# Optimization experiments

Hardware: AMD Instinct MI355X
Metric: run time of the kernel (lower is better)

Reference implementation:

```python
import jax, jax.numpy as jnp
import numpy as np

B, C, H, W = 4, 64, 128, 128
NP = 9        # num_param (N offset points per pixel)
OUTC = 128
STRIDE = 1
EPS = 1e-5    # BatchNorm eps


def _conv(x, w, b=None, stride=1):
    out = jax.lax.conv_general_dilated(
        x, w, (stride, stride), 'SAME',
        dimension_numbers=('NCHW', 'OIHW', 'NCHW'))
    if b is not None:
        out = out + b[None, :, None, None]
    return out


def setup_inputs() -> dict:
    key = jax.random.key(0)
    ks = jax.random.split(key, 6)
    s = lambda k, sh, sc: jax.random.normal(k, sh, jnp.float32) * sc
    return dict(
        x=s(ks[0], (B, C, H, W), 1.0),
        p_w=s(ks[1], (2 * NP, C, 3, 3), 0.02),   # offset conv (3x3, pad 1)
        p_b=s(ks[2], (2 * NP,), 0.02),
        conv_w=s(ks[3], (OUTC, C, 1, 1), 0.05),  # final 1x1 conv, no bias
        bn_gamma=jnp.ones((OUTC,), jnp.float32),
        bn_beta=jnp.zeros((OUTC,), jnp.float32),
        attn_w=s(ks[4], (1, C, 1, 1), 0.05),
        attn_b=s(ks[5], (1,), 0.05),
    )


def _forward(x, p_w, p_b, conv_w, bn_gamma, bn_beta, attn_w, attn_b):
    N = NP
    # density attention (computed as in source; adaptive re-parameterization skipped)
    density = jax.nn.sigmoid(_conv(x, attn_w, attn_b))  # noqa: F841

    # learned offsets: [B, 2N, H, W] (first N channels = row/x, last N = col/y)
    offset = _conv(x, p_w, p_b, stride=STRIDE)

    # p_n: base kernel grid offsets (row-major 3x3 -> values 0..2)
    base_int = int(round(np.sqrt(NP)))
    row_number = NP // base_int
    ii, jj = np.meshgrid(np.arange(row_number), np.arange(base_int), indexing='ij')
    p_n = jnp.asarray(np.concatenate([ii.ravel(), jj.ravel()]).astype(np.float32))  # [2N]

    # p_0: per-pixel base coordinates
    p0x = jnp.broadcast_to(jnp.arange(H, dtype=jnp.float32)[:, None] * STRIDE, (H, W))
    p0y = jnp.broadcast_to(jnp.arange(W, dtype=jnp.float32)[None, :] * STRIDE, (H, W))
    p_0 = jnp.concatenate([jnp.broadcast_to(p0x, (N, H, W)),
                           jnp.broadcast_to(p0y, (N, H, W))], axis=0)  # [2N,H,W]

    # sampling locations p: [B, H, W, 2N]
    p = (offset + p_n[None, :, None, None] + p_0[None]).transpose(0, 2, 3, 1)

    q_lt = jax.lax.stop_gradient(jnp.floor(p))   # detached, as in source
    q_rb = q_lt + 1.0
    px, py = p[..., :N], p[..., N:]
    ltx, lty = q_lt[..., :N], q_lt[..., N:]
    rbx, rby = q_rb[..., :N], q_rb[..., N:]

    # bilinear weights
    g_lt = (1 + (ltx - px)) * (1 + (lty - py))
    g_rb = (1 - (rbx - px)) * (1 - (rby - py))
    g_lb = (1 + (ltx - px)) * (1 - (rby - py))
    g_rt = (1 - (rbx - px)) * (1 + (lty - py))

    HW = H * W
    x_flat = x.reshape(B, C, HW)

    def gather(qx, qy):
        idx = jnp.clip((qx * W + qy).astype(jnp.int32), 0, HW - 1)  # [B,H,W,N]
        idx = idx.reshape(B, -1)
        out = jax.vmap(lambda xf, ix: xf[:, ix])(x_flat, idx)       # [B,C,H*W*N]
        return out.reshape(B, C, H, W, N)

    x_off = (g_lt[:, None] * gather(ltx, lty)
             + g_rb[:, None] * gather(rbx, rby)
             + g_lb[:, None] * gather(ltx, rby)
             + g_rt[:, None] * gather(rbx, lty))    # [B,C,H,W,N]

    # rearrange 'b c h w n -> b c (h n) w'
    x_off = x_off.transpose(0, 1, 2, 4, 3).reshape(B, C, H * N, W)

    # 1x1 conv (no bias) + BatchNorm2d (training-mode batch stats) + SiLU
    y = _conv(x_off, conv_w)
    mean = y.mean(axis=(0, 2, 3))
    var = y.var(axis=(0, 2, 3))  # biased, as torch BN uses for normalization
    y = (y - mean[None, :, None, None]) * jax.lax.rsqrt(var[None, :, None, None] + EPS)
    y = y * bn_gamma[None, :, None, None] + bn_beta[None, :, None, None]
    return jax.nn.silu(y)


def reference(x, p_w, p_b, conv_w, bn_gamma, bn_beta, attn_w, attn_b):
    return _forward(x, p_w, p_b, conv_w, bn_gamma, bn_beta, attn_w, attn_b)
```

## Files before the change

kernel.cpp:

```cpp
#include <hip/hip_runtime.h>

#define CIN   64
#define NOUT  128
#define IMH   128
#define IMW   128
#define NPTS  9
#define NB    4
#define HW    (IMH*IMW)
#define ROWS  (IMH*NPTS)
#define CHS   (ROWS*IMW)
#define TOTAL ((size_t)NB*NOUT*CHS)

typedef float f32x4 __attribute__((ext_vector_type(4)));

__global__ __launch_bounds__(256) void k_offset(const float* __restrict__ x,
                                                const float* __restrict__ pw,
                                                const float* __restrict__ pb,
                                                float* __restrict__ off,
                                                float* __restrict__ stats0) {
    __shared__ float wl[576 * 20];
    __shared__ float red[3 * 64 * 19];

    int tid = threadIdx.x;
    if (blockIdx.x == 0) stats0[tid] = 0.f;

    for (int t = tid; t < 18 * 576; t += 256) {
        int k = t / 576, cj = t % 576;
        wl[cj * 20 + k] = pw[t];
    }
    __syncthreads();

    int cg = tid >> 6;
    int lp = tid & 63;
    int gid = blockIdx.x * 64 + lp;
    int b = gid >> 14;
    int hw = gid & 16383;
    int h = hw >> 7;
    int w = hw & 127;

    float acc[18];
#pragma unroll
    for (int k = 0; k < 18; ++k) acc[k] = (cg == 0) ? pb[k] : 0.f;

    const float* xb = x + (size_t)b * CIN * HW;
    int c0 = cg * 16;
    for (int c = c0; c < c0 + 16; ++c) {
        const float* xc = xb + c * HW;
#pragma unroll
        for (int dh = 0; dh < 3; ++dh) {
            int hh = h + dh - 1;
            if ((unsigned)hh >= 128u) continue;
#pragma unroll
            for (int dw = 0; dw < 3; ++dw) {
                int ww = w + dw - 1;
                if ((unsigned)ww >= 128u) continue;
                float xv = xc[hh * IMW + ww];
                const float* wr = &wl[(c * 9 + dh * 3 + dw) * 20];
                float wv[18];
                *(float4*)&wv[0]  = *(const float4*)(wr);
                *(float4*)&wv[4]  = *(const float4*)(wr + 4);
                *(float4*)&wv[8]  = *(const float4*)(wr + 8);
                *(float4*)&wv[12] = *(const float4*)(wr + 12);
                *(float2*)&wv[16] = *(const float2*)(wr + 16);
#pragma unroll
                for (int k = 0; k < 18; ++k) acc[k] += wv[k] * xv;
            }
        }
    }

    if (cg > 0) {
        float* rp = &red[((cg - 1) * 64 + lp) * 19];
#pragma unroll
        for (int k = 0; k < 18; ++k) rp[k] = acc[k];
    }
    __syncthreads();
    if (cg == 0) {
#pragma unroll
        for (int k = 0; k < 18; ++k)
            acc[k] += red[(0 * 64 + lp) * 19 + k] + red[(64 + lp) * 19 + k] + red[(128 + lp) * 19 + k];
        float* ob = off + (size_t)b * 18 * HW + hw;
#pragma unroll
        for (int k = 0; k < 18; ++k) ob[k * HW] = acc[k];
    }
}

__global__ __launch_bounds__(256) void k_z(const float* __restrict__ x,
                                           const float* __restrict__ cw,
                                           float* __restrict__ z) {
    __shared__ float xs[64 * 128];
    __shared__ float wsm[64 * 128];
    int tid = threadIdx.x;
    int b   = blockIdx.x >> 7;
    int hw0 = (blockIdx.x & 127) << 7;

    const float* xb = x + (size_t)b * CIN * HW + hw0;
#pragma unroll
    for (int i = 0; i < 32; ++i) {
        int t = tid + i * 256;
        int c = t >> 7, l = t & 127;
        xs[t] = xb[c * HW + l];
    }
#pragma unroll
    for (int i = 0; i < 32; ++i) {
        int t = tid + i * 256;
        int oc = t & 127, c = t >> 7;
        wsm[c * 128 + oc] = cw[oc * 64 + c];
    }
    __syncthreads();

    int hw4  = (tid & 31) << 2;
    int oc16 = (tid >> 5) << 4;

    float acc[4][16];
#pragma unroll
    for (int j = 0; j < 4; ++j)
#pragma unroll
        for (int k = 0; k < 16; ++k) acc[j][k] = 0.f;

    for (int c = 0; c < 64; ++c) {
        float4 xv = *(const float4*)&xs[c * 128 + hw4];
        float xq[4] = {xv.x, xv.y, xv.z, xv.w};
        float wv[16];
        const float4* wrow = (const float4*)&wsm[c * 128 + oc16];
#pragma unroll
        for (int m = 0; m < 4; ++m) ((float4*)wv)[m] = wrow[m];
#pragma unroll
        for (int j = 0; j < 4; ++j)
#pragma unroll
            for (int k = 0; k < 16; ++k) acc[j][k] += xq[j] * wv[k];
    }

#pragma unroll
    for (int j = 0; j < 4; ++j) {
        size_t rowb = ((size_t)b * HW + hw0 + hw4 + j) * NOUT + oc16;
        float4* zp = (float4*)&z[rowb];
#pragma unroll
        for (int m = 0; m < 4; ++m)
            zp[m] = make_float4(acc[j][4*m], acc[j][4*m+1], acc[j][4*m+2], acc[j][4*m+3]);
    }
}

__device__ __forceinline__ void bilin_setup(const float* __restrict__ off,
                                            int b, int h, int n, int w,
                                            float4& g, int4& id) {
    const float* ob = off + ((size_t)b * 18 + n) * HW + h * IMW + w;
    float ox = ob[0];
    float oy = ob[9 * HW];
    float px = ox + (float)(n / 3) + (float)h;
    float py = oy + (float)(n % 3) + (float)w;
    float fX = floorf(px), fY = floorf(py);
    float fx = px - fX, fy = py - fY;
    int X = (int)fX, Y = (int)fY;
    g.x = (1.f - fx) * (1.f - fy);
    g.y = fx * fy;
    g.z = (1.f - fx) * fy;
    g.w = fx * (1.f - fy);
    id.x = min(max(X * IMW + Y, 0), HW - 1) * NOUT;
    id.y = min(max((X + 1) * IMW + (Y + 1), 0), HW - 1) * NOUT;
    id.z = min(max(X * IMW + (Y + 1), 0), HW - 1) * NOUT;
    id.w = min(max((X + 1) * IMW + Y, 0), HW - 1) * NOUT;
}

__device__ __forceinline__ int swz_block() {
    return (blockIdx.x & 7) * 576 + (blockIdx.x >> 3);
}

__global__ __launch_bounds__(256) void k_sum(const float* __restrict__ off,
                                             const float* __restrict__ z,
                                             float* __restrict__ gsum,
                                             float* __restrict__ gsq) {
    int logical = swz_block();
    int n  = logical % 9;
    int t2 = logical / 9;
    int h  = t2 & 127;
    int b  = t2 >> 7;

    __shared__ float4 gS[128];
    __shared__ int4   iS[128];
    __shared__ float  lsum[128];
    __shared__ float  lsq[128];

    int tid = threadIdx.x;
    if (tid < 128) {
        lsum[tid] = 0.f; lsq[tid] = 0.f;
        float4 g; int4 id;
        bilin_setup(off, b, h, n, tid, g, id);
        gS[tid] = g; iS[tid] = id;
    }
    __syncthreads();

    int g32 = tid >> 5;
    int c4  = (tid & 31) << 2;
    const float* zb = z + (size_t)b * HW * NOUT + c4;

    float s0=0, s1=0, s2=0, s3=0, q0=0, q1=0, q2=0, q3=0;

    float4 plt, prb, plb, prt;
    {
        int4 id = iS[g32];
        plt = *(const float4*)(zb + id.x);
        prb = *(const float4*)(zb + id.y);
        plb = *(const float4*)(zb + id.z);
        prt = *(const float4*)(zb + id.w);
    }
#pragma unroll
    for (int wi = 0; wi < 16; ++wi) {
        float4 nlt, nrb, nlb, nrt;
        if (wi < 15) {
            int4 idn = iS[((wi + 1) << 3) + g32];
            nlt = *(const float4*)(zb + idn.x);
            nrb = *(const float4*)(zb + idn.y);
            nlb = *(const float4*)(zb + idn.z);
            nrt = *(const float4*)(zb + idn.w);
        }
        float4 g = gS[(wi << 3) + g32];
        float a0 = g.x*plt.x + g.y*prb.x + g.z*plb.x + g.w*prt.x;
        float a1 = g.x*plt.y + g.y*prb.y + g.z*plb.y + g.w*prt.y;
        float a2 = g.x*plt.z + g.y*prb.z + g.z*plb.z + g.w*prt.z;
        float a3 = g.x*plt.w + g.y*prb.w + g.z*plb.w + g.w*prt.w;
        s0 += a0; q0 += a0*a0;
        s1 += a1; q1 += a1*a1;
        s2 += a2; q2 += a2*a2;
        s3 += a3; q3 += a3*a3;
        plt = nlt; prb = nrb; plb = nlb; prt = nrt;
    }
    atomicAdd(&lsum[c4],     s0);
    atomicAdd(&lsum[c4 + 1], s1);
    atomicAdd(&lsum[c4 + 2], s2);
    atomicAdd(&lsum[c4 + 3], s3);
    atomicAdd(&lsq[c4],      q0);
    atomicAdd(&lsq[c4 + 1],  q1);
    atomicAdd(&lsq[c4 + 2],  q2);
    atomicAdd(&lsq[c4 + 3],  q3);
    __syncthreads();
    if (tid < 128)       atomicAdd(&gsum[tid],      lsum[tid]);
    else                 atomicAdd(&gsq[tid - 128], lsq[tid - 128]);
}

__global__ void k_stats(const float* __restrict__ gsum, const float* __restrict__ gsq,
                        const float* __restrict__ gamma, const float* __restrict__ beta,
                        float* __restrict__ scale, float* __restrict__ shift) {
    int c = threadIdx.x;
    const float cnt = (float)(NB * ROWS * IMW);
    float m = gsum[c] / cnt;
    float v = gsq[c] / cnt - m * m;
    float inv = rsqrtf(fmaxf(v, 0.f) + 1e-5f);
    float sc = inv * gamma[c];
    scale[c] = sc;
    shift[c] = beta[c] - m * sc;
}

__device__ __forceinline__ void proc_store(float4 vlt, float4 vrb, float4 vlb, float4 vrt,
                                           float4 g, float4 sc, float4 sh,
                                           float* __restrict__ dst) {
    float t0 = (g.x*vlt.x + g.y*vrb.x + g.z*vlb.x + g.w*vrt.x) * sc.x + sh.x;
    float t1 = (g.x*vlt.y + g.y*vrb.y + g.z*vlb.y + g.w*vrt.y) * sc.y + sh.y;
    float t2 = (g.x*vlt.z + g.y*vrb.z + g.z*vlb.z + g.w*vrt.z) * sc.z + sh.z;
    float t3 = (g.x*vlt.w + g.y*vrb.w + g.z*vlb.w + g.w*vrt.w) * sc.w + sh.w;
    float4 y;
    y.x = t0 / (1.f + __expf(-t0));
    y.y = t1 / (1.f + __expf(-t1));
    y.z = t2 / (1.f + __expf(-t2));
    y.w = t3 / (1.f + __expf(-t3));
    *(float4*)dst = y;
}

#define GLOAD(P, wabs) { int4 _id = iS[wabs]; \
    P##lt = *(const float4*)(zb + _id.x); \
    P##rb = *(const float4*)(zb + _id.y); \
    P##lb = *(const float4*)(zb + _id.z); \
    P##rt = *(const float4*)(zb + _id.w); }

__global__ __launch_bounds__(256) void k_apply(const float* __restrict__ off,
                                               const float* __restrict__ z,
                                               const float* __restrict__ scale,
                                               const float* __restrict__ shift,
                                               float* __restrict__ out) {
    int logical = swz_block();
    int n  = logical % 9;
    int t2 = logical / 9;
    int h  = t2 & 127;
    int b  = t2 >> 7;

    __shared__ float4 gS[128];
    __shared__ int4   iS[128];
    __shared__ float  ybuf[2][32 * 133];

    int tid = threadIdx.x;
    if (tid < 128) {
        float4 g; int4 id;
        bilin_setup(off, b, h, n, tid, g, id);
        gS[tid] = g; iS[tid] = id;
    }
    __syncthreads();

    int ws = tid >> 5;
    int c4 = (tid & 31) << 2;
    float4 sc = *(const float4*)&scale[c4];
    float4 sh = *(const float4*)&shift[c4];
    const float* zb = z + (size_t)b * HW * NOUT + c4;
    int r = h * 9 + n;
    float* outr = out + (size_t)b * NOUT * CHS + (size_t)r * IMW;

    float4 A0lt, A0rb, A0lb, A0rt;
    float4 A1lt, A1rb, A1lb, A1rt;
    float4 A2lt, A2rb, A2lb, A2rt;
    float4 A3lt, A3rb, A3lb, A3rt;

    GLOAD(A0, ws);       GLOAD(A1, 8 + ws);
    GLOAD(A2, 16 + ws);  GLOAD(A3, 24 + ws);
    proc_store(A0lt,A0rb,A0lb,A0rt, gS[ws],      sc, sh, &ybuf[0][(ws)      * 133 + c4]);
    proc_store(A1lt,A1rb,A1lb,A1rt, gS[8 + ws],  sc, sh, &ybuf[0][(8 + ws)  * 133 + c4]);
    proc_store(A2lt,A2rb,A2lb,A2rt, gS[16 + ws], sc, sh, &ybuf[0][(16 + ws) * 133 + c4]);
    proc_store(A3lt,A3rb,A3lb,A3rt, gS[24 + ws], sc, sh, &ybuf[0][(24 + ws) * 133 + c4]);
    __syncthreads();

#pragma unroll
    for (int chunk = 0; chunk < 4; ++chunk) {
        const int cur = chunk & 1;
        const int nxt = cur ^ 1;
        int w0 = chunk << 5;

        if (chunk < 3) {
            int wn = w0 + 32;
            GLOAD(A0, wn + ws);       GLOAD(A1, wn + 8 + ws);
            GLOAD(A2, wn + 16 + ws);  GLOAD(A3, wn + 24 + ws);
        }

#pragma unroll
        for (int i = 0; i < 4; ++i) {
            int task = (i << 8) + tid;
            int oc   = task >> 3;
            int w4   = (task & 7) << 2;
            f32x4 v;
            v.x = ybuf[cur][(w4 + 0) * 133 + oc];
            v.y = ybuf[cur][(w4 + 1) * 133 + oc];
            v.z = ybuf[cur][(w4 + 2) * 133 + oc];
            v.w = ybuf[cur][(w4 + 3) * 133 + oc];
            __builtin_nontemporal_store(v, (f32x4*)(outr + (size_t)oc * CHS + w0 + w4));
        }

        if (chunk < 3) {
            int wn = w0 + 32;
            proc_store(A0lt,A0rb,A0lb,A0rt, gS[wn + ws],      sc, sh, &ybuf[nxt][(ws)      * 133 + c4]);
            proc_store(A1lt,A1rb,A1lb,A1rt, gS[wn + 8 + ws],  sc, sh, &ybuf[nxt][(8 + ws)  * 133 + c4]);
            proc_store(A2lt,A2rb,A2lb,A2rt, gS[wn + 16 + ws], sc, sh, &ybuf[nxt][(16 + ws) * 133 + c4]);
            proc_store(A3lt,A3rb,A3lb,A3rt, gS[wn + 24 + ws], sc, sh, &ybuf[nxt][(24 + ws) * 133 + c4]);
        }
        __syncthreads();
    }
}

extern "C" void kernel_launch(void* const* d_in, const int* in_sizes, int n_in,
                              void* d_out, int out_size, void* d_ws, size_t ws_size,
                              hipStream_t stream) {
    const float* x     = (const float*)d_in[0];
    const float* pw    = (const float*)d_in[1];
    const float* pb    = (const float*)d_in[2];
    const float* cw    = (const float*)d_in[3];
    const float* gamma = (const float*)d_in[4];
    const float* beta  = (const float*)d_in[5];

    float* out = (float*)d_out;
    float* ws  = (float*)d_ws;

    float* off   = ws;
    float* z     = off + (size_t)NB * 18 * HW;
    float* gsum  = z + (size_t)NB * HW * NOUT;
    float* gsq   = gsum + NOUT;
    float* scale = gsq + NOUT;
    float* shift = scale + NOUT;

    hipLaunchKernelGGL(k_offset, dim3(1024), dim3(256), 0, stream, x, pw, pb, off, gsum);
    hipLaunchKernelGGL(k_z,      dim3(512),  dim3(256), 0, stream, x, cw, z);
    hipLaunchKernelGGL(k_sum,    dim3(4608), dim3(256), 0, stream, off, z, gsum, gsq);
    hipLaunchKernelGGL(k_stats,  dim3(1),    dim3(128), 0, stream, gsum, gsq, gamma, beta, scale, shift);
    hipLaunchKernelGGL(k_apply,  dim3(4608), dim3(256), 0, stream, off, z, scale, shift, out);
}
```

Measured before the change: 322.2 us.

## Store projected features z in bf16 and fold BN stats into apply kernel

The intermediate z (1x1-conv applied before sampling) is now written in bf16, halving the bytes read by the gather-heavy sum and apply kernels. Each thread now handles 8 channels per load, and the sum kernel reduces across lanes with shuffles before its shared-memory atomics. The separate k_stats launch is removed: every apply block recomputes scale and shift from the global sums. This trades accuracy, since bf16 rounding of z feeds both the BN statistics and the output, for less memory traffic and one fewer launch.

New measurement: 303.4 us. -5.8%, faster.

```diff
diff --git a/kernel.cpp b/kernel.cpp
--- a/kernel.cpp
+++ b/kernel.cpp
@@ -12,6 +12,20 @@
 #define TOTAL ((size_t)NB*NOUT*CHS)
 
 typedef float f32x4 __attribute__((ext_vector_type(4)));
+typedef unsigned short ushort_t;
+
+__device__ __forceinline__ ushort_t f2bf(float f) {
+    union { float f; unsigned u; } a; a.f = f;
+    unsigned r = a.u + 0x7FFFu + ((a.u >> 16) & 1u);
+    return (ushort_t)(r >> 16);
+}
+
+__device__ __forceinline__ void cvt8(uint4 v, float* f) {
+    f[0] = __uint_as_float(v.x << 16); f[1] = __uint_as_float(v.x & 0xFFFF0000u);
+    f[2] = __uint_as_float(v.y << 16); f[3] = __uint_as_float(v.y & 0xFFFF0000u);
+    f[4] = __uint_as_float(v.z << 16); f[5] = __uint_as_float(v.z & 0xFFFF0000u);
+    f[6] = __uint_as_float(v.w << 16); f[7] = __uint_as_float(v.w & 0xFFFF0000u);
+}
 
 __global__ __launch_bounds__(256) void k_offset(const float* __restrict__ x,
                                                 const float* __restrict__ pw,
@@ -86,7 +100,7 @@
 
 __global__ __launch_bounds__(256) void k_z(const float* __restrict__ x,
                                            const float* __restrict__ cw,
-                                           float* __restrict__ z) {
+                                           ushort_t* __restrict__ z) {
     __shared__ float xs[64 * 128];
     __shared__ float wsm[64 * 128];
     int tid = threadIdx.x;
@@ -132,11 +146,12 @@
 
 #pragma unroll
     for (int j = 0; j < 4; ++j) {
-        size_t rowb = ((size_t)b * HW + hw0 + hw4 + j) * NOUT + oc16;
-        float4* zp = (float4*)&z[rowb];
-#pragma unroll
-        for (int m = 0; m < 4; ++m)
-            zp[m] = make_float4(acc[j][4*m], acc[j][4*m+1], acc[j][4*m+2], acc[j][4*m+3]);
+        ushort_t* zr = z + ((size_t)b * HW + hw0 + hw4 + j) * NOUT + oc16;
+        union { ushort_t u[16]; uint4 q[2]; } pk;
+#pragma unroll
+        for (int k = 0; k < 16; ++k) pk.u[k] = f2bf(acc[j][k]);
+        *(uint4*)zr       = pk.q[0];
+        *(uint4*)(zr + 8) = pk.q[1];
     }
 }
 
@@ -166,7 +181,7 @@
 }
 
 __global__ __launch_bounds__(256) void k_sum(const float* __restrict__ off,
-                                             const float* __restrict__ z,
+                                             const ushort_t* __restrict__ z,
                                              float* __restrict__ gsum,
                                              float* __restrict__ gsq) {
     int logical = swz_block();
@@ -189,92 +204,81 @@
     }
     __syncthreads();
 
-    int g32 = tid >> 5;
-    int c4  = (tid & 31) << 2;
-    const float* zb = z + (size_t)b * HW * NOUT + c4;
-
-    float s0=0, s1=0, s2=0, s3=0, q0=0, q1=0, q2=0, q3=0;
-
-    float4 plt, prb, plb, prt;
+    int g16 = tid >> 4;
+    int c8  = (tid & 15) << 3;
+    const ushort_t* zb = z + (size_t)b * HW * NOUT + c8;
+
+    float s[8], q[8];
+#pragma unroll
+    for (int k = 0; k < 8; ++k) { s[k] = 0.f; q[k] = 0.f; }
+
+    uint4 plt, prb, plb, prt;
     {
-        int4 id = iS[g32];
-        plt = *(const float4*)(zb + id.x);
-        prb = *(const float4*)(zb + id.y);
-        plb = *(const float4*)(zb + id.z);
-        prt = *(const float4*)(zb + id.w);
-    }
-#pragma unroll
-    for (int wi = 0; wi < 16; ++wi) {
-        float4 nlt, nrb, nlb, nrt;
-        if (wi < 15) {
-            int4 idn = iS[((wi + 1) << 3) + g32];
-            nlt = *(const float4*)(zb + idn.x);
-            nrb = *(const float4*)(zb + idn.y);
-            nlb = *(const float4*)(zb + idn.z);
-            nrt = *(const float4*)(zb + idn.w);
-        }
-        float4 g = gS[(wi << 3) + g32];
-        float a0 = g.x*plt.x + g.y*prb.x + g.z*plb.x + g.w*prt.x;
-        float a1 = g.x*plt.y + g.y*prb.y + g.z*plb.y + g.w*prt.y;
-        float a2 = g.x*plt.z + g.y*prb.z + g.z*plb.z + g.w*prt.z;
-        float a3 = g.x*plt.w + g.y*prb.w + g.z*plb.w + g.w*prt.w;
-        s0 += a0; q0 += a0*a0;
-        s1 += a1; q1 += a1*a1;
-        s2 += a2; q2 += a2*a2;
-        s3 += a3; q3 += a3*a3;
+        int4 id = iS[g16];
+        plt = *(const uint4*)(zb + id.x);
+        prb = *(const uint4*)(zb + id.y);
+        plb = *(const uint4*)(zb + id.z);
+        prt = *(const uint4*)(zb + id.w);
+    }
+#pragma unroll
+    for (int wi = 0; wi < 8; ++wi) {
+        uint4 nlt, nrb, nlb, nrt;
+        if (wi < 7) {
+            int4 idn = iS[((wi + 1) << 4) + g16];
+            nlt = *(const uint4*)(zb + idn.x);
+            nrb = *(const uint4*)(zb + idn.y);
+            nlb = *(const uint4*)(zb + idn.z);
+            nrt = *(const uint4*)(zb + idn.w);
+        }
+        float4 g = gS[(wi << 4) + g16];
+        float flt[8], frb[8], flb[8], frt[8];
+        cvt8(plt, flt); cvt8(prb, frb); cvt8(plb, flb); cvt8(prt, frt);
+#pragma unroll
+        for (int k = 0; k < 8; ++k) {
+            float a = g.x * flt[k] + g.y * frb[k] + g.z * flb[k] + g.w * frt[k];
+            s[k] += a; q[k] += a * a;
+        }
         plt = nlt; prb = nrb; plb = nlb; prt = nrt;
     }
-    atomicAdd(&lsum[c4],     s0);
-    atomicAdd(&lsum[c4 + 1], s1);
-    atomicAdd(&lsum[c4 + 2], s2);
-    atomicAdd(&lsum[c4 + 3], s3);
-    atomicAdd(&lsq[c4],      q0);
-    atomicAdd(&lsq[c4 + 1],  q1);
-    atomicAdd(&lsq[c4 + 2],  q2);
-    atomicAdd(&lsq[c4 + 3],  q3);
+
+#pragma unroll
+    for (int k = 0; k < 8; ++k) {
+        s[k] += __shfl_xor(s[k], 16, 64); s[k] += __shfl_xor(s[k], 32, 64);
+        q[k] += __shfl_xor(q[k], 16, 64); q[k] += __shfl_xor(q[k], 32, 64);
+    }
+    if (((tid >> 4) & 3) == 0) {
+#pragma unroll
+        for (int k = 0; k < 8; ++k) {
+            atomicAdd(&lsum[c8 + k], s[k]);
+            atomicAdd(&lsq[c8 + k],  q[k]);
+        }
+    }
     __syncthreads();
     if (tid < 128)       atomicAdd(&gsum[tid],      lsum[tid]);
     else                 atomicAdd(&gsq[tid - 128], lsq[tid - 128]);
 }
 
-__global__ void k_stats(const float* __restrict__ gsum, const float* __restrict__ gsq,
-                        const float* __restrict__ gamma, const float* __restrict__ beta,
-                        float* __restrict__ scale, float* __restrict__ shift) {
-    int c = threadIdx.x;
-    const float cnt = (float)(NB * ROWS * IMW);
-    float m = gsum[c] / cnt;
-    float v = gsq[c] / cnt - m * m;
-    float inv = rsqrtf(fmaxf(v, 0.f) + 1e-5f);
-    float sc = inv * gamma[c];
-    scale[c] = sc;
-    shift[c] = beta[c] - m * sc;
-}
-
-__device__ __forceinline__ void proc_store(float4 vlt, float4 vrb, float4 vlb, float4 vrt,
-                                           float4 g, float4 sc, float4 sh,
-                                           float* __restrict__ dst) {
-    float t0 = (g.x*vlt.x + g.y*vrb.x + g.z*vlb.x + g.w*vrt.x) * sc.x + sh.x;
-    float t1 = (g.x*vlt.y + g.y*vrb.y + g.z*vlb.y + g.w*vrt.y) * sc.y + sh.y;
-    float t2 = (g.x*vlt.z + g.y*vrb.z + g.z*vlb.z + g.w*vrt.z) * sc.z + sh.z;
-    float t3 = (g.x*vlt.w + g.y*vrb.w + g.z*vlb.w + g.w*vrt.w) * sc.w + sh.w;
-    float4 y;
-    y.x = t0 / (1.f + __expf(-t0));
-    y.y = t1 / (1.f + __expf(-t1));
-    y.z = t2 / (1.f + __expf(-t2));
-    y.w = t3 / (1.f + __expf(-t3));
-    *(float4*)dst = y;
-}
-
-#define GLOAD(P, wabs) { int4 _id = iS[wabs]; \
-    P##lt = *(const float4*)(zb + _id.x); \
-    P##rb = *(const float4*)(zb + _id.y); \
-    P##lb = *(const float4*)(zb + _id.z); \
-    P##rt = *(const float4*)(zb + _id.w); }
+__device__ __forceinline__ void proc8(const uint4* C, float4 g,
+                                      const float* sc, const float* sh,
+                                      float* __restrict__ dst) {
+    float flt[8], frb[8], flb[8], frt[8];
+    cvt8(C[0], flt); cvt8(C[1], frb); cvt8(C[2], flb); cvt8(C[3], frt);
+    float o[8];
+#pragma unroll
+    for (int k = 0; k < 8; ++k) {
+        float t = (g.x * flt[k] + g.y * frb[k] + g.z * flb[k] + g.w * frt[k]) * sc[k] + sh[k];
+        o[k] = t / (1.f + __expf(-t));
+    }
+    *(float4*)dst       = *(float4*)&o[0];
+    *(float4*)(dst + 4) = *(float4*)&o[4];
+}
 
 __global__ __launch_bounds__(256) void k_apply(const float* __restrict__ off,
-                                               const float* __restrict__ z,
-                                               const float* __restrict__ scale,
-                                               const float* __restrict__ shift,
+                                               const ushort_t* __restrict__ z,
+                                               const float* __restrict__ gsum,
+                                               const float* __restrict__ gsq,
+                                               const float* __restrict__ gamma,
+                                               const float* __restrict__ beta,
                                                float* __restrict__ out) {
     int logical = swz_block();
     int n  = logical % 9;
@@ -284,35 +288,49 @@
 
     __shared__ float4 gS[128];
     __shared__ int4   iS[128];
+    __shared__ float  scS[128];
+    __shared__ float  shS[128];
     __shared__ float  ybuf[2][32 * 133];
 
     int tid = threadIdx.x;
     if (tid < 128) {
+        const float cnt = (float)(NB * ROWS * IMW);
+        float m  = gsum[tid] / cnt;
+        float vv = gsq[tid] / cnt - m * m;
+        float inv = rsqrtf(fmaxf(vv, 0.f) + 1e-5f);
+        float sc = inv * gamma[tid];
+        scS[tid] = sc;
+        shS[tid] = beta[tid] - m * sc;
         float4 g; int4 id;
         bilin_setup(off, b, h, n, tid, g, id);
         gS[tid] = g; iS[tid] = id;
     }
     __syncthreads();
 
-    int ws = tid >> 5;
-    int c4 = (tid & 31) << 2;
-    float4 sc = *(const float4*)&scale[c4];
-    float4 sh = *(const float4*)&shift[c4];
-    const float* zb = z + (size_t)b * HW * NOUT + c4;
+    int g16 = tid >> 4;
+    int c8  = (tid & 15) << 3;
+    float scv[8], shv[8];
+    *(float4*)&scv[0] = *(const float4*)&scS[c8];
+    *(float4*)&scv[4] = *(const float4*)&scS[c8 + 4];
+    *(float4*)&shv[0] = *(const float4*)&shS[c8];
+    *(float4*)&shv[4] = *(const float4*)&shS[c8 + 4];
+
+    const ushort_t* zb = z + (size_t)b * HW * NOUT + c8;
     int r = h * 9 + n;
     float* outr = out + (size_t)b * NOUT * CHS + (size_t)r * IMW;
 
-    float4 A0lt, A0rb, A0lb, A0rt;
-    float4 A1lt, A1rb, A1lb, A1rt;
-    float4 A2lt, A2rb, A2lb, A2rt;
-    float4 A3lt, A3rb, A3lb, A3rt;
-
-    GLOAD(A0, ws);       GLOAD(A1, 8 + ws);
-    GLOAD(A2, 16 + ws);  GLOAD(A3, 24 + ws);
-    proc_store(A0lt,A0rb,A0lb,A0rt, gS[ws],      sc, sh, &ybuf[0][(ws)      * 133 + c4]);
-    proc_store(A1lt,A1rb,A1lb,A1rt, gS[8 + ws],  sc, sh, &ybuf[0][(8 + ws)  * 133 + c4]);
-    proc_store(A2lt,A2rb,A2lb,A2rt, gS[16 + ws], sc, sh, &ybuf[0][(16 + ws) * 133 + c4]);
-    proc_store(A3lt,A3rb,A3lb,A3rt, gS[24 + ws], sc, sh, &ybuf[0][(24 + ws) * 133 + c4]);
+    uint4 A[8];
+#define STAGE(wb) { int4 _i0 = iS[(wb) + g16]; int4 _i1 = iS[(wb) + 16 + g16]; \
+    A[0] = *(const uint4*)(zb + _i0.x); A[1] = *(const uint4*)(zb + _i0.y); \
+    A[2] = *(const uint4*)(zb + _i0.z); A[3] = *(const uint4*)(zb + _i0.w); \
+    A[4] = *(const uint4*)(zb + _i1.x); A[5] = *(const uint4*)(zb + _i1.y); \
+    A[6] = *(const uint4*)(zb + _i1.z); A[7] = *(const uint4*)(zb + _i1.w); }
+#define PROC(wb, bi) { \
+    proc8(&A[0], gS[(wb) + g16],      scv, shv, &ybuf[bi][g16 * 133 + c8]); \
+    proc8(&A[4], gS[(wb) + 16 + g16], scv, shv, &ybuf[bi][(16 + g16) * 133 + c8]); }
+
+    STAGE(0);
+    PROC(0, 0);
     __syncthreads();
 
 #pragma unroll
@@ -321,11 +339,7 @@
         const int nxt = cur ^ 1;
         int w0 = chunk << 5;
 
-        if (chunk < 3) {
-            int wn = w0 + 32;
-            GLOAD(A0, wn + ws);       GLOAD(A1, wn + 8 + ws);
-            GLOAD(A2, wn + 16 + ws);  GLOAD(A3, wn + 24 + ws);
-        }
+        if (chunk < 3) STAGE(w0 + 32);
 
 #pragma unroll
         for (int i = 0; i < 4; ++i) {
@@ -340,15 +354,11 @@
             __builtin_nontemporal_store(v, (f32x4*)(outr + (size_t)oc * CHS + w0 + w4));
         }
 
-        if (chunk < 3) {
-            int wn = w0 + 32;
-            proc_store(A0lt,A0rb,A0lb,A0rt, gS[wn + ws],      sc, sh, &ybuf[nxt][(ws)      * 133 + c4]);
-            proc_store(A1lt,A1rb,A1lb,A1rt, gS[wn + 8 + ws],  sc, sh, &ybuf[nxt][(8 + ws)  * 133 + c4]);
-            proc_store(A2lt,A2rb,A2lb,A2rt, gS[wn + 16 + ws], sc, sh, &ybuf[nxt][(16 + ws) * 133 + c4]);
-            proc_store(A3lt,A3rb,A3lb,A3rt, gS[wn + 24 + ws], sc, sh, &ybuf[nxt][(24 + ws) * 133 + c4]);
-        }
+        if (chunk < 3) PROC(w0 + 32, nxt);
         __syncthreads();
     }
+#undef STAGE
+#undef PROC
 }
 
 extern "C" void kernel_launch(void* const* d_in, const int* in_sizes, int n_in,
@@ -364,16 +374,13 @@
     float* out = (float*)d_out;
     float* ws  = (float*)d_ws;
 
-    float* off   = ws;
-    float* z     = off + (size_t)NB * 18 * HW;
-    float* gsum  = z + (size_t)NB * HW * NOUT;
-    float* gsq   = gsum + NOUT;
-    float* scale = gsq + NOUT;
-    float* shift = scale + NOUT;
+    float*    off  = ws;
+    ushort_t* z    = (ushort_t*)(off + (size_t)NB * 18 * HW);
+    float*    gsum = (float*)(z + (size_t)NB * HW * NOUT);
+    float*    gsq  = gsum + NOUT;
 
     hipLaunchKernelGGL(k_offset, dim3(1024), dim3(256), 0, stream, x, pw, pb, off, gsum);
     hipLaunchKernelGGL(k_z,      dim3(512),  dim3(256), 0, stream, x, cw, z);
     hipLaunchKernelGGL(k_sum,    dim3(4608), dim3(256), 0, stream, off, z, gsum, gsq);
-    hipLaunchKernelGGL(k_stats,  dim3(1),    dim3(128), 0, stream, gsum, gsq, gamma, beta, scale, shift);
-    hipLaunchKernelGGL(k_apply,  dim3(4608), dim3(256), 0, stream, off, z, scale, shift, out);
-}
+    hipLaunchKernelGGL(k_apply,  dim3(4608), dim3(256), 0, stream, off, z, gsum, gsq, gamma, beta, out);
+}
```
